# Kernel optimization log

Hardware: AMD Instinct MI355X
Metric: run time of the kernel (lower is better)

The kernel has to match this reference:

```python
import jax, jax.numpy as jnp
import numpy as np

NUM_BANDS, B, K, D = 5, 512, 64, 200
H = 4            # num attention heads
HID = 512        # selector hidden width
S = 0.02         # weight init scale


def setup_inputs() -> dict:
    key = jax.random.key(0)
    ks = jax.random.split(key, 8)
    F_IN = NUM_BANDS * K * D  # 64000
    return {
        "bands": jax.random.normal(ks[0], (NUM_BANDS, B, K, D), jnp.float32),
        "w1": jax.random.normal(ks[1], (HID, F_IN), jnp.float32) * S,
        "b1": jnp.zeros((HID,), jnp.float32),
        "w2": jax.random.normal(ks[2], (NUM_BANDS, HID), jnp.float32) * S,
        "b2": jnp.zeros((NUM_BANDS,), jnp.float32),
        "in_proj_w": jax.random.normal(ks[3], (3 * D, D), jnp.float32) * S,
        "in_proj_b": jnp.zeros((3 * D,), jnp.float32),
        "out_w": jax.random.normal(ks[4], (D, D), jnp.float32) * S,
        "out_b": jnp.zeros((D,), jnp.float32),
    }


def reference(bands, w1, b1, w2, b2, in_proj_w, in_proj_b, out_w, out_b):
    nb, Bb, k, d = bands.shape
    hd = d // H
    scale = 1.0 / np.sqrt(hd)

    # concat(bands, dim=1): [B, nb*k, d] in band-major order
    x = jnp.transpose(bands, (1, 0, 2, 3))           # [B, nb, k, d]
    kv_in = x.reshape(Bb, nb * k, d)                 # [B, nb*k, d]

    # router MLP + softmax + argmax band select
    flat = kv_in.reshape(Bb, -1)                     # [B, nb*k*d]
    h = jax.nn.relu(flat @ w1.T + b1)                # [B, HID]
    band_weights = jax.nn.softmax(h @ w2.T + b2, axis=-1)
    sel = jnp.argmax(band_weights, axis=-1)          # [B] int

    # gather selected band per sample as the query
    Q = bands[sel, jnp.arange(Bb)]                   # [B, k, d]

    # multihead cross-attention (torch nn.MultiheadAttention math)
    wq, wk, wv = jnp.split(in_proj_w, 3, axis=0)
    bq, bk, bv = jnp.split(in_proj_b, 3, axis=0)
    q = (Q @ wq.T + bq).reshape(Bb, k, H, hd).transpose(0, 2, 1, 3)        # [B,H,k,hd]
    kk = (kv_in @ wk.T + bk).reshape(Bb, nb * k, H, hd).transpose(0, 2, 1, 3)
    v = (kv_in @ wv.T + bv).reshape(Bb, nb * k, H, hd).transpose(0, 2, 1, 3)

    attn = jax.nn.softmax(jnp.einsum('bhqe,bhke->bhqk', q, kk) * scale, axis=-1)
    o = jnp.einsum('bhqk,bhke->bhqe', attn, v)       # [B,H,k,hd]
    o = o.transpose(0, 2, 1, 3).reshape(Bb, k, d)
    return o @ out_w.T + out_b                        # [B, k, d]
```

## Files before the change

### kernel.cpp

```cpp
#include <hip/hip_runtime.h>
#include <hip/hip_bf16.h>

#define NBANDS 5
#define BATCH  512
#define KQN    64
#define DM     200
#define NHEAD  4
#define HD     50
#define HIDW   512
#define TKV    320
#define FIN    64000
#define BSTRIDE 6553600
#define KSPLIT 40
#define KCH    1600
#define RCH    25
#define NTT    13
#define KST    7
#define NTKV   25

typedef __bf16  bf16x8 __attribute__((ext_vector_type(8)));
typedef float   f32x4  __attribute__((ext_vector_type(4)));

static __device__ inline unsigned short f2bf(float f) {
    __hip_bfloat16 h = __float2bfloat16(f);
    return *reinterpret_cast<unsigned short*>(&h);
}
static __device__ inline float bf2f(unsigned short u) {
    union { unsigned int i; float f; } x;
    x.i = ((unsigned int)u) << 16;
    return x.f;
}
static __device__ inline bf16x8 bf8zero() {
    union { bf16x8 v; unsigned int u[4]; } z;
    z.u[0] = z.u[1] = z.u[2] = z.u[3] = 0u;
    return z.v;
}
static __device__ inline void split8(const float4& a, const float4& b,
                                     bf16x8& hi, bf16x8& lo) {
    union { bf16x8 v; unsigned short u[8]; } H, L;
    const float xs[8] = {a.x, a.y, a.z, a.w, b.x, b.y, b.z, b.w};
#pragma unroll
    for (int i = 0; i < 8; ++i) {
        H.u[i] = f2bf(xs[i]);
        L.u[i] = f2bf(xs[i] - bf2f(H.u[i]));
    }
    hi = H.v; lo = L.v;
}
static __device__ inline bf16x8 round8(const float4& a, const float4& b) {
    union { bf16x8 v; unsigned short u[8]; } H;
    const float xs[8] = {a.x, a.y, a.z, a.w, b.x, b.y, b.z, b.w};
#pragma unroll
    for (int i = 0; i < 8; ++i) H.u[i] = f2bf(xs[i]);
    return H.v;
}

__global__ __launch_bounds__(256) void k_splitw1(
    const float* __restrict__ w1, unsigned short* __restrict__ BHp,
    unsigned short* __restrict__ BLp)
{
    __shared__ __align__(16) unsigned short Hs[128][72];
    __shared__ __align__(16) unsigned short Ls[128][72];
    const int kc = blockIdx.x;
    const int jt = blockIdx.y;
    const int t  = threadIdx.x;
    const int rl0 = t >> 4, cl4 = (t & 15) * 4;
#pragma unroll
    for (int i = 0; i < 8; ++i) {
        const int row = rl0 + i * 16;
        const float4 v = *(const float4*)(w1
            + (size_t)(jt * 128 + row) * FIN + kc * 64 + cl4);
        ushort4 hh, ll;
        hh.x = f2bf(v.x); ll.x = f2bf(v.x - bf2f(hh.x));
        hh.y = f2bf(v.y); ll.y = f2bf(v.y - bf2f(hh.y));
        hh.z = f2bf(v.z); ll.z = f2bf(v.z - bf2f(hh.z));
        hh.w = f2bf(v.w); ll.w = f2bf(v.w - bf2f(hh.w));
        *(ushort4*)&Hs[row][cl4] = hh;
        *(ushort4*)&Ls[row][cl4] = ll;
    }
    __syncthreads();
    const size_t tbase = ((size_t)(jt * 1000 + kc)) << 13;
#pragma unroll
    for (int i = 0; i < 4; ++i) {
        const int slot = i * 256 + t;
        const int ksnt = slot >> 6, lane = slot & 63;
        const int ks = ksnt >> 3, nt = ksnt & 7;
        const int row = nt * 16 + (lane & 15);
        const int col = ks * 32 + (lane >> 4) * 8;
        *(uint4*)(BHp + tbase + (size_t)slot * 8) = *(const uint4*)&Hs[row][col];
        *(uint4*)(BLp + tbase + (size_t)slot * 8) = *(const uint4*)&Ls[row][col];
    }
}

__global__ __launch_bounds__(256, 2) void k_router_mfma(
    const float* __restrict__ bands, const unsigned short* __restrict__ BHp,
    const unsigned short* __restrict__ BLp, float* __restrict__ part)
{
    __shared__ __align__(16) unsigned short BsH[2][8192];
    __shared__ __align__(16) unsigned short BsL[2][8192];

    const int lin = (blockIdx.z << 5) | (blockIdx.y << 2) | blockIdx.x;
    const int logical = (lin & 7) * 160 + (lin >> 3);
    const int z   = logical >> 5;
    const int rem = logical & 31;
    const int bt  = rem >> 2, jt = rem & 3;
    const int b0  = bt << 6, j0 = jt << 7;

    const int t = threadIdx.x;
    const int w = t >> 6, lane = t & 63;
    const int lm = lane & 15, quad = lane >> 4;
    const int m0 = w << 4;

    const float* xrow = bands + (size_t)(z >> 3) * BSTRIDE
                      + (size_t)(b0 + m0 + lm) * 12800 + (z & 7) * KCH
                      + quad * 8;
    const size_t tile0 = ((size_t)(jt * 1000 + z * RCH)) << 13;

    auto stage = [&](int chunk, int buf) {
        const unsigned short* srcH = BHp + tile0 + ((size_t)chunk << 13);
        const unsigned short* srcL = BLp + tile0 + ((size_t)chunk << 13);
#pragma unroll
        for (int pass = 0; pass < 4; ++pass) {
            const int i = pass * 256 + t;
            __builtin_amdgcn_global_load_lds(
                (const __attribute__((address_space(1))) unsigned int*)(srcH + (size_t)i * 8),
                (__attribute__((address_space(3))) unsigned int*)&BsH[buf][(pass * 256 + w * 64) * 8],
                16, 0, 0);
            __builtin_amdgcn_global_load_lds(
                (const __attribute__((address_space(1))) unsigned int*)(srcL + (size_t)i * 8),
                (__attribute__((address_space(3))) unsigned int*)&BsL[buf][(pass * 256 + w * 64) * 8],
                16, 0, 0);
        }
    };

    f32x4 acc[8];
#pragma unroll
    for (int nt = 0; nt < 8; ++nt) acc[nt] = (f32x4){0.f, 0.f, 0.f, 0.f};

    stage(0, 0);
    __syncthreads();
    for (int chunk = 0; chunk < RCH; ++chunk) {
        const int buf = chunk & 1;
        if (chunk + 1 < RCH) stage(chunk + 1, buf ^ 1);
        const float* ap = xrow + chunk * 64;
        const float4 a00 = *(const float4*)(ap);
        const float4 a01 = *(const float4*)(ap + 4);
        const float4 a10 = *(const float4*)(ap + 32);
        const float4 a11 = *(const float4*)(ap + 36);
        bf16x8 ah0, al0, ah1, al1;
        split8(a00, a01, ah0, al0);
        split8(a10, a11, ah1, al1);
        const unsigned short* hc = &BsH[buf][lane * 8];
        const unsigned short* lc = &BsL[buf][lane * 8];
#pragma unroll
        for (int nt = 0; nt < 8; ++nt) {
            const bf16x8 bh = *(const bf16x8*)(hc + (nt << 9));
            const bf16x8 bl = *(const bf16x8*)(lc + (nt << 9));
            acc[nt] = __builtin_amdgcn_mfma_f32_16x16x32_bf16(ah0, bh, acc[nt], 0, 0, 0);
            acc[nt] = __builtin_amdgcn_mfma_f32_16x16x32_bf16(al0, bh, acc[nt], 0, 0, 0);
            acc[nt] = __builtin_amdgcn_mfma_f32_16x16x32_bf16(ah0, bl, acc[nt], 0, 0, 0);
        }
#pragma unroll
        for (int nt = 0; nt < 8; ++nt) {
            const bf16x8 bh = *(const bf16x8*)(hc + ((8 + nt) << 9));
            const bf16x8 bl = *(const bf16x8*)(lc + ((8 + nt) << 9));
            acc[nt] = __builtin_amdgcn_mfma_f32_16x16x32_bf16(ah1, bh, acc[nt], 0, 0, 0);
            acc[nt] = __builtin_amdgcn_mfma_f32_16x16x32_bf16(al1, bh, acc[nt], 0, 0, 0);
            acc[nt] = __builtin_amdgcn_mfma_f32_16x16x32_bf16(ah1, bl, acc[nt], 0, 0, 0);
        }
        __syncthreads();
    }
    float* po = part + (size_t)z * (BATCH * HIDW);
#pragma unroll
    for (int nt = 0; nt < 8; ++nt) {
        const int jj = j0 + nt * 16 + lm;
#pragma unroll
        for (int reg = 0; reg < 4; ++reg) {
            const int bb = b0 + m0 + quad * 4 + reg;
            po[(size_t)bb * HIDW + jj] = acc[nt][reg];
        }
    }
}

__global__ __launch_bounds__(256) void k_reduce_relu(
    const float* __restrict__ part, const float* __restrict__ b1,
    float* __restrict__ h)
{
    const int tid = blockIdx.x * 256 + threadIdx.x;
    float s = b1[tid & (HIDW - 1)];
#pragma unroll 8
    for (int z = 0; z < KSPLIT; ++z) s += part[z * (BATCH * HIDW) + tid];
    h[tid] = fmaxf(s, 0.f);
}

__global__ __launch_bounds__(256) void k_wpack(
    const float* __restrict__ ipw, const float* __restrict__ outw,
    unsigned short* __restrict__ WqHp, unsigned short* __restrict__ WqLp,
    unsigned short* __restrict__ OwHp, unsigned short* __restrict__ OwLp)
{
    const int p = blockIdx.x;
    const int ks = p / NTT, nt = p - ks * NTT;
    const int t = threadIdx.x;
    const int lane = t >> 2, e0 = (t & 3) * 2;
    const int lm = lane & 15, quad = lane >> 4;
    const int row = nt * 16 + lm;
    const int k  = ks * 32 + quad * 8 + e0;
    const float* src = (blockIdx.y == 0) ? ipw : outw;
    unsigned short* dh = (blockIdx.y == 0) ? WqHp : OwHp;
    unsigned short* dl = (blockIdx.y == 0) ? WqLp : OwLp;
    float v0 = 0.f, v1 = 0.f;
    if (row < DM && k < DM) {
        v0 = src[(size_t)row * DM + k];
        v1 = src[(size_t)row * DM + k + 1];
    }
    const int off = (p << 9) + (lane << 3) + e0;
    const unsigned short h0 = f2bf(v0), h1 = f2bf(v1);
    dh[off]     = h0;
    dh[off + 1] = h1;
    dl[off]     = f2bf(v0 - bf2f(h0));
    dl[off + 1] = f2bf(v1 - bf2f(h1));
}

__global__ __launch_bounds__(256) void k_wpack_kv(
    const float* __restrict__ ipw, unsigned short* __restrict__ Wkv)
{
    const int p = blockIdx.x;
    const int ks = p / NTKV, nt = p - ks * NTKV;
    const int t = threadIdx.x;
    const int lane = t >> 2, e0 = (t & 3) * 2;
    const int lm = lane & 15, quad = lane >> 4;
    const int row = nt * 16 + lm;
    const int k  = ks * 32 + quad * 8 + e0;
    float v0 = 0.f, v1 = 0.f;
    if (k < DM) {
        v0 = ipw[(size_t)(DM + row) * DM + k];
        v1 = ipw[(size_t)(DM + row) * DM + k + 1];
    }
    const int off = (p << 9) + (lane << 3) + e0;
    Wkv[off]     = f2bf(v0);
    Wkv[off + 1] = f2bf(v1);
}

__global__ __launch_bounds__(256) void k_argmax(
    const float* __restrict__ h, const float* __restrict__ w2,
    const float* __restrict__ b2, int* __restrict__ sel)
{
    __shared__ float red[NBANDS][256];
    const int b = blockIdx.x, t = threadIdx.x;
    float acc[NBANDS] = {0.f, 0.f, 0.f, 0.f, 0.f};
    for (int j = t; j < HIDW; j += 256) {
        const float hv = h[b * HIDW + j];
#pragma unroll
        for (int n = 0; n < NBANDS; ++n)
            acc[n] = fmaf(hv, w2[n * HIDW + j], acc[n]);
    }
#pragma unroll
    for (int n = 0; n < NBANDS; ++n) red[n][t] = acc[n];
    __syncthreads();
    for (int s = 128; s > 0; s >>= 1) {
        if (t < s) {
#pragma unroll
            for (int n = 0; n < NBANDS; ++n) red[n][t] += red[n][t + s];
        }
        __syncthreads();
    }
    if (t == 0) {
        int best = 0;
        float bv = red[0][0] + b2[0];
        for (int n = 1; n < NBANDS; ++n) {
            const float v = red[n][0] + b2[n];
            if (v > bv) { bv = v; best = n; }
        }
        sel[b] = best;
    }
}

template<bool BF16OUT>
static __device__ inline void proj_core(
    const float* __restrict__ x0,
    const unsigned short* __restrict__ Ph,
    const unsigned short* __restrict__ Pl,
    const float* __restrict__ bias,
    void* __restrict__ outp)
{
    const int t = threadIdx.x;
    const int w = t >> 6, lane = t & 63;
    const int lm = lane & 15, quad = lane >> 4;
    const int m0 = w * 16;
    const float* xrow = x0 + (size_t)(m0 + lm) * DM;

    f32x4 acc[NTT];
#pragma unroll
    for (int nt = 0; nt < NTT; ++nt) acc[nt] = (f32x4){0.f, 0.f, 0.f, 0.f};

#pragma unroll
    for (int ks = 0; ks < KST; ++ks) {
        const int k0 = ks * 32 + quad * 8;
        bf16x8 a_h = bf8zero(), a_l = bf8zero();
        if (k0 + 8 <= DM) {
            const float4 xa = *(const float4*)(xrow + k0);
            const float4 xb = *(const float4*)(xrow + k0 + 4);
            split8(xa, xb, a_h, a_l);
        }
        const unsigned short* ph = Ph + ((ks * NTT) << 9) + (lane << 3);
        const unsigned short* pl = Pl + ((ks * NTT) << 9) + (lane << 3);
#pragma unroll
        for (int nt = 0; nt < NTT; ++nt) {
            const bf16x8 b_h = *(const bf16x8*)(ph + (nt << 9));
            const bf16x8 b_l = *(const bf16x8*)(pl + (nt << 9));
            acc[nt] = __builtin_amdgcn_mfma_f32_16x16x32_bf16(a_h, b_h, acc[nt], 0, 0, 0);
            acc[nt] = __builtin_amdgcn_mfma_f32_16x16x32_bf16(a_l, b_h, acc[nt], 0, 0, 0);
            acc[nt] = __builtin_amdgcn_mfma_f32_16x16x32_bf16(a_h, b_l, acc[nt], 0, 0, 0);
        }
    }
#pragma unroll
    for (int nt = 0; nt < NTT; ++nt) {
        const int col = nt * 16 + lm;
        if (col < DM) {
            const float bs = bias[col];
#pragma unroll
            for (int reg = 0; reg < 4; ++reg) {
                const int row = m0 + quad * 4 + reg;
                const float v = acc[nt][reg] + bs;
                if (BF16OUT)
                    ((unsigned short*)outp)[(size_t)row * DM + col] = f2bf(v);
                else
                    ((float*)outp)[(size_t)row * DM + col] = v;
            }
        }
    }
}

__global__ __launch_bounds__(256) void k_qproj_mfma(
    const float* __restrict__ bands, const int* __restrict__ sel,
    const unsigned short* __restrict__ WqHp, const unsigned short* __restrict__ WqLp,
    const float* __restrict__ ipb, unsigned short* __restrict__ qb)
{
    const int b = blockIdx.x;
    const int band = sel[b];
    const float* x0 = bands + (size_t)((band * BATCH + b) * KQN) * DM;
    proj_core<true>(x0, WqHp, WqLp, ipb, qb + (size_t)(b * KQN) * DM);
}

__global__ __launch_bounds__(256) void k_outproj_mfma(
    const float* __restrict__ obuf, const unsigned short* __restrict__ OwHp,
    const unsigned short* __restrict__ OwLp, const float* __restrict__ outb,
    float* __restrict__ out)
{
    const int b = blockIdx.x;
    proj_core<false>(obuf + (size_t)(b * KQN) * DM, OwHp, OwLp, outb,
                     out + (size_t)(b * KQN) * DM);
}

__global__ __launch_bounds__(256) void k_kvproj_lds(
    const float* __restrict__ bands, const unsigned short* __restrict__ Wkv,
    const float* __restrict__ ipb, __hip_bfloat16* __restrict__ Kp,
    __hip_bfloat16* __restrict__ Vp)
{
    __shared__ __align__(16) unsigned short Bs[2][NTKV * 512];
    const int t = threadIdx.x;
    const int w = t >> 6, lane = t & 63;
    const int lm = lane & 15, quad = lane >> 4;
    const int m0 = w * 16;
    const int M0 = blockIdx.x * 64;

    const int gg = M0 + m0 + lm;
    const int bb = gg / TKV, tk = gg - bb * TKV;
    const int band = tk >> 6, kk = tk & 63;
    const float* xrow = bands + (size_t)((band * BATCH + bb) * KQN + kk) * DM;

    float4 ar[2 * KST];
#pragma unroll
    for (int ks = 0; ks < KST; ++ks) {
        const int k0 = ks * 32 + quad * 8;
        if (k0 + 8 <= DM) {
            ar[2 * ks]     = *(const float4*)(xrow + k0);
            ar[2 * ks + 1] = *(const float4*)(xrow + k0 + 4);
        }
    }
    bf16x8 a[KST];
#pragma unroll
    for (int ks = 0; ks < KST; ++ks) {
        const int k0 = ks * 32 + quad * 8;
        a[ks] = (k0 + 8 <= DM) ? round8(ar[2 * ks], ar[2 * ks + 1]) : bf8zero();
    }

    auto stage = [&](int ks, int buf) {
        const unsigned short* src = Wkv + ((ks * NTKV) << 9);
#pragma unroll
        for (int pass = 0; pass < 6; ++pass) {
            const int i = pass * 256 + t;
            __builtin_amdgcn_global_load_lds(
                (const __attribute__((address_space(1))) unsigned int*)(src + (size_t)i * 8),
                (__attribute__((address_space(3))) unsigned int*)&Bs[buf][(pass * 256 + w * 64) * 8],
                16, 0, 0);
        }
        if (t < 64) {
            __builtin_amdgcn_global_load_lds(
                (const __attribute__((address_space(1))) unsigned int*)(src + (size_t)(1536 + lane) * 8),
                (__attribute__((address_space(3))) unsigned int*)&Bs[buf][1536 * 8],
                16, 0, 0);
        }
    };

    f32x4 acc[NTKV];
#pragma unroll
    for (int nt = 0; nt < NTKV; ++nt) acc[nt] = (f32x4){0.f, 0.f, 0.f, 0.f};

    stage(0, 0);
    __syncthreads();
#pragma unroll
    for (int ks = 0; ks < KST; ++ks) {
        if (ks + 1 < KST) stage(ks + 1, (ks + 1) & 1);
        const unsigned short* bs = &Bs[ks & 1][lane * 8];
#pragma unroll
        for (int nt = 0; nt < NTKV; ++nt) {
            const bf16x8 b8 = *(const bf16x8*)(bs + (nt << 9));
            acc[nt] = __builtin_amdgcn_mfma_f32_16x16x32_bf16(a[ks], b8, acc[nt], 0, 0, 0);
        }
        __syncthreads();
    }

#pragma unroll
    for (int nt = 0; nt < NTKV; ++nt) {
        const int col = nt * 16 + lm;
        const float bias = ipb[DM + col];
#pragma unroll
        for (int reg = 0; reg < 4; ++reg) {
            const int grow = M0 + m0 + quad * 4 + reg;
            const float v = acc[nt][reg] + bias;
            if (col < DM) Kp[(size_t)grow * DM + col] = __float2bfloat16(v);
            else          Vp[(size_t)grow * DM + (col - DM)] = __float2bfloat16(v);
        }
    }
}

__global__ __launch_bounds__(256) void k_attn(
    const unsigned short* __restrict__ qb, const __hip_bfloat16* __restrict__ Kp,
    const __hip_bfloat16* __restrict__ Vp, float* __restrict__ obuf)
{
    __shared__ __align__(16) unsigned short Qs[64][72];
    __shared__ __align__(16) unsigned short KP[320][72];
    __shared__ __align__(16) unsigned short Vt[64][328];
    __shared__ __align__(16) unsigned short Ps[64][328];
    const int b = blockIdx.x, hh = blockIdx.y;
    const int t = threadIdx.x;

    const unsigned short* qbase = qb + (size_t)(b * KQN) * DM + hh * HD;
    for (int idx = t; idx < 64 * 64; idx += 256) {
        const int r = idx >> 6, e = idx & 63;
        Qs[r][e] = (e < HD) ? qbase[(size_t)r * DM + e] : 0;
    }
    const unsigned short* kbase = (const unsigned short*)Kp + (size_t)b * TKV * DM + hh * HD;
    for (int idx = t; idx < 320 * 25; idx += 256) {
        const int key = idx / 25, g = idx - key * 25;
        *(unsigned int*)&KP[key][g * 2] =
            *(const unsigned int*)(kbase + (size_t)key * DM + g * 2);
    }
    for (int idx = t; idx < 320 * 7; idx += 256) {
        const int key = idx / 7, g = idx - key * 7;
        *(unsigned int*)&KP[key][50 + g * 2] = 0;
    }
    const unsigned short* vbase = (const unsigned short*)Vp + (size_t)b * TKV * DM + hh * HD;
    for (int idx = t; idx < 320 * 25; idx += 256) {
        const int key = idx / 25, g = idx - key * 25;
        const unsigned int v = *(const unsigned int*)(vbase + (size_t)key * DM + g * 2);
        Vt[g * 2][key]     = (unsigned short)(v & 0xffffu);
        Vt[g * 2 + 1][key] = (unsigned short)(v >> 16);
    }
    __syncthreads();

    const int w = t >> 6, lane = t & 63;
    const int lm = lane & 15, quad = lane >> 4;
    const int m0 = w * 16;

    f32x4 s[20];
#pragma unroll
    for (int nt = 0; nt < 20; ++nt) s[nt] = (f32x4){0.f, 0.f, 0.f, 0.f};
#pragma unroll
    for (int ks = 0; ks < 2; ++ks) {
        const int ka = ks * 32 + quad * 8;
        const bf16x8 a = *(const bf16x8*)&Qs[m0 + lm][ka];
#pragma unroll
        for (int nt = 0; nt < 20; ++nt) {
            const bf16x8 bb8 = *(const bf16x8*)&KP[nt * 16 + lm][ka];
            s[nt] = __builtin_amdgcn_mfma_f32_16x16x32_bf16(a, bb8, s[nt], 0, 0, 0);
        }
    }

    const float scale = 0.14142135623730951f;
    float inv[4];
#pragma unroll
    for (int reg = 0; reg < 4; ++reg) {
        float mx = -1e30f;
#pragma unroll
        for (int nt = 0; nt < 20; ++nt) {
            const float sv = s[nt][reg] * scale;
            s[nt][reg] = sv;
            mx = fmaxf(mx, sv);
        }
#pragma unroll
        for (int off = 1; off < 16; off <<= 1)
            mx = fmaxf(mx, __shfl_xor(mx, off, 64));
        float lsum = 0.f;
#pragma unroll
        for (int nt = 0; nt < 20; ++nt) {
            const float p = __expf(s[nt][reg] - mx);
            s[nt][reg] = p;
            lsum += p;
        }
#pragma unroll
        for (int off = 1; off < 16; off <<= 1)
            lsum += __shfl_xor(lsum, off, 64);
        inv[reg] = 1.f / lsum;
    }
#pragma unroll
    for (int reg = 0; reg < 4; ++reg) {
        const int row = m0 + quad * 4 + reg;
#pragma unroll
        for (int nt = 0; nt < 20; ++nt)
            Ps[row][nt * 16 + lm] = f2bf(s[nt][reg]);
    }
    __syncthreads();

    f32x4 o[4];
#pragma unroll
    for (int nt = 0; nt < 4; ++nt) o[nt] = (f32x4){0.f, 0.f, 0.f, 0.f};
#pragma unroll
    for (int ks = 0; ks < 10; ++ks) {
        const int ka = ks * 32 + quad * 8;
        const bf16x8 a = *(const bf16x8*)&Ps[m0 + lm][ka];
#pragma unroll
        for (int nt = 0; nt < 4; ++nt) {
            const bf16x8 bb8 = *(const bf16x8*)&Vt[nt * 16 + lm][ka];
            o[nt] = __builtin_amdgcn_mfma_f32_16x16x32_bf16(a, bb8, o[nt], 0, 0, 0);
        }
    }
    float* op = obuf + (size_t)(b * KQN) * DM + hh * HD;
#pragma unroll
    for (int nt = 0; nt < 4; ++nt) {
        const int e = nt * 16 + lm;
        if (e < HD) {
#pragma unroll
            for (int reg = 0; reg < 4; ++reg) {
                const int row = m0 + quad * 4 + reg;
                op[(size_t)row * DM + e] = o[nt][reg] * inv[reg];
            }
        }
    }
}

extern "C" void kernel_launch(void* const* d_in, const int* in_sizes, int n_in,
                              void* d_out, int out_size, void* d_ws, size_t ws_size,
                              hipStream_t stream)
{
    const float* bands = (const float*)d_in[0];
    const float* w1    = (const float*)d_in[1];
    const float* b1    = (const float*)d_in[2];
    const float* w2    = (const float*)d_in[3];
    const float* b2    = (const float*)d_in[4];
    const float* ipw   = (const float*)d_in[5];
    const float* ipb   = (const float*)d_in[6];
    const float* outw  = (const float*)d_in[7];
    const float* outb  = (const float*)d_in[8];
    float* out = (float*)d_out;

    if (ws_size < (size_t)192940032) return;

    char* ws = (char*)d_ws;
    int*   sel  = (int*)  (ws + 0);
    unsigned short* BHp  = (unsigned short*)(ws + 4096);
    unsigned short* BLp  = (unsigned short*)(ws + 65540096);
    float* part = (float*)(ws + 131076096);
    float* h    = (float*)(ws + 173019136);
    unsigned short* qb   = (unsigned short*)(ws + 4096);
    __hip_bfloat16* Kp   = (__hip_bfloat16*)(ws + 26776832);
    __hip_bfloat16* Vp   = (__hip_bfloat16*)(ws + 92312832);
    float* obuf = (float*)(ws + 157848832);
    unsigned short* Wkv  = (unsigned short*)(ws + 184063232);
    unsigned short* WqHp = (unsigned short*)(ws + 184242432);
    unsigned short* WqLp = (unsigned short*)(ws + 184335616);
    unsigned short* OwHp = (unsigned short*)(ws + 184428800);
    unsigned short* OwLp = (unsigned short*)(ws + 184521984);

    k_wpack_kv<<<KST * NTKV, 256, 0, stream>>>(ipw, Wkv);
    k_wpack<<<dim3(KST * NTT, 2), 256, 0, stream>>>(ipw, outw, WqHp, WqLp, OwHp, OwLp);
    k_splitw1<<<dim3(1000, 4), 256, 0, stream>>>(w1, BHp, BLp);

    k_router_mfma<<<dim3(4, 8, KSPLIT), 256, 0, stream>>>(bands, BHp, BLp, part);
    k_reduce_relu<<<(BATCH * HIDW) / 256, 256, 0, stream>>>(part, b1, h);
    k_argmax<<<BATCH, 256, 0, stream>>>(h, w2, b2, sel);
    k_qproj_mfma<<<BATCH, 256, 0, stream>>>(bands, sel, WqHp, WqLp, ipb, qb);
    k_kvproj_lds<<<2560, 256, 0, stream>>>(bands, Wkv, ipb, Kp, Vp);
    k_attn<<<dim3(BATCH, NHEAD), 256, 0, stream>>>(qb, Kp, Vp, obuf);
    k_outproj_mfma<<<BATCH, 256, 0, stream>>>(obuf, OwHp, OwLp, outb, out);
}
```

Baseline: 870.6 us.

## Retile router GEMM to 128x128 block tiles with 2x2 warp layout

Changes the router MFMA kernel from 64-row by 128-column tiles to 128x128 tiles. Each warp now computes a 64x64 sub-tile (4 row-subtiles by 4 column-subtiles), and the K loop advances 32 elements per stage with half-size LDS buffers. Doubling the rows per block halves the number of blocks and reuses each staged w1 tile across twice as many batch rows, cutting global and LDS traffic for the weights. In exchange, each thread holds more accumulator registers and the launch bound is raised to 3 blocks per CU, which risks register spills or lower occupancy.

```diff
diff --git a/kernel.cpp b/kernel.cpp
--- a/kernel.cpp
+++ b/kernel.cpp
@@ -13,7 +13,7 @@
 #define BSTRIDE 6553600
 #define KSPLIT 40
 #define KCH    1600
-#define RCH    25
+#define RC32   50
 #define NTT    13
 #define KST    7
 #define NTKV   25
@@ -91,92 +91,97 @@
     }
 }
 
-__global__ __launch_bounds__(256, 2) void k_router_mfma(
+__global__ __launch_bounds__(256, 3) void k_router_mfma(
     const float* __restrict__ bands, const unsigned short* __restrict__ BHp,
     const unsigned short* __restrict__ BLp, float* __restrict__ part)
 {
-    __shared__ __align__(16) unsigned short BsH[2][8192];
-    __shared__ __align__(16) unsigned short BsL[2][8192];
-
-    const int lin = (blockIdx.z << 5) | (blockIdx.y << 2) | blockIdx.x;
-    const int logical = (lin & 7) * 160 + (lin >> 3);
-    const int z   = logical >> 5;
-    const int rem = logical & 31;
+    __shared__ __align__(16) unsigned short BsH[2][4096];
+    __shared__ __align__(16) unsigned short BsL[2][4096];
+
+    const int lin = (blockIdx.z << 4) | (blockIdx.y << 2) | blockIdx.x;
+    const int logical = (lin & 7) * 80 + (lin >> 3);
+    const int z   = logical >> 4;
+    const int rem = logical & 15;
     const int bt  = rem >> 2, jt = rem & 3;
-    const int b0  = bt << 6, j0 = jt << 7;
 
     const int t = threadIdx.x;
     const int w = t >> 6, lane = t & 63;
     const int lm = lane & 15, quad = lane >> 4;
-    const int m0 = w << 4;
-
-    const float* xrow = bands + (size_t)(z >> 3) * BSTRIDE
-                      + (size_t)(b0 + m0 + lm) * 12800 + (z & 7) * KCH
-                      + quad * 8;
-    const size_t tile0 = ((size_t)(jt * 1000 + z * RCH)) << 13;
-
-    auto stage = [&](int chunk, int buf) {
-        const unsigned short* srcH = BHp + tile0 + ((size_t)chunk << 13);
-        const unsigned short* srcL = BLp + tile0 + ((size_t)chunk << 13);
-#pragma unroll
-        for (int pass = 0; pass < 4; ++pass) {
+    const int wr = w >> 1, wc = w & 1;
+
+    const float* xbase = bands + (size_t)(z >> 3) * BSTRIDE
+                       + (size_t)(bt * 128 + wr * 64 + lm) * 12800
+                       + (z & 7) * KCH + quad * 8;
+    const unsigned short* hbase = BHp + ((size_t)(jt * 1000 + z * 25) << 13);
+    const unsigned short* lbase = BLp + ((size_t)(jt * 1000 + z * 25) << 13);
+
+    auto stage = [&](int c, int buf) {
+        const size_t off = ((size_t)(c >> 1) << 13) + ((size_t)(c & 1) << 12);
+        const unsigned short* sH = hbase + off;
+        const unsigned short* sL = lbase + off;
+#pragma unroll
+        for (int pass = 0; pass < 2; ++pass) {
             const int i = pass * 256 + t;
             __builtin_amdgcn_global_load_lds(
-                (const __attribute__((address_space(1))) unsigned int*)(srcH + (size_t)i * 8),
+                (const __attribute__((address_space(1))) unsigned int*)(sH + (size_t)i * 8),
                 (__attribute__((address_space(3))) unsigned int*)&BsH[buf][(pass * 256 + w * 64) * 8],
                 16, 0, 0);
             __builtin_amdgcn_global_load_lds(
-                (const __attribute__((address_space(1))) unsigned int*)(srcL + (size_t)i * 8),
+                (const __attribute__((address_space(1))) unsigned int*)(sL + (size_t)i * 8),
                 (__attribute__((address_space(3))) unsigned int*)&BsL[buf][(pass * 256 + w * 64) * 8],
                 16, 0, 0);
         }
     };
 
-    f32x4 acc[8];
-#pragma unroll
-    for (int nt = 0; nt < 8; ++nt) acc[nt] = (f32x4){0.f, 0.f, 0.f, 0.f};
+    f32x4 acc[4][4];
+#pragma unroll
+    for (int rs = 0; rs < 4; ++rs)
+#pragma unroll
+        for (int nt = 0; nt < 4; ++nt) acc[rs][nt] = (f32x4){0.f, 0.f, 0.f, 0.f};
 
     stage(0, 0);
     __syncthreads();
-    for (int chunk = 0; chunk < RCH; ++chunk) {
-        const int buf = chunk & 1;
-        if (chunk + 1 < RCH) stage(chunk + 1, buf ^ 1);
-        const float* ap = xrow + chunk * 64;
-        const float4 a00 = *(const float4*)(ap);
-        const float4 a01 = *(const float4*)(ap + 4);
-        const float4 a10 = *(const float4*)(ap + 32);
-        const float4 a11 = *(const float4*)(ap + 36);
-        bf16x8 ah0, al0, ah1, al1;
-        split8(a00, a01, ah0, al0);
-        split8(a10, a11, ah1, al1);
-        const unsigned short* hc = &BsH[buf][lane * 8];
-        const unsigned short* lc = &BsL[buf][lane * 8];
-#pragma unroll
-        for (int nt = 0; nt < 8; ++nt) {
+    for (int c = 0; c < RC32; ++c) {
+        const int buf = c & 1;
+        if (c + 1 < RC32) stage(c + 1, buf ^ 1);
+        float4 a0[4], a1[4];
+#pragma unroll
+        for (int rs = 0; rs < 4; ++rs) {
+            const float* ap = xbase + (size_t)(rs * 16) * 12800 + c * 32;
+            a0[rs] = *(const float4*)(ap);
+            a1[rs] = *(const float4*)(ap + 4);
+        }
+        bf16x8 ah[4], al[4];
+#pragma unroll
+        for (int rs = 0; rs < 4; ++rs) split8(a0[rs], a1[rs], ah[rs], al[rs]);
+        const unsigned short* hc = &BsH[buf][(wc * 4) * 512 + lane * 8];
+        const unsigned short* lc = &BsL[buf][(wc * 4) * 512 + lane * 8];
+#pragma unroll
+        for (int nt = 0; nt < 4; ++nt) {
             const bf16x8 bh = *(const bf16x8*)(hc + (nt << 9));
             const bf16x8 bl = *(const bf16x8*)(lc + (nt << 9));
-            acc[nt] = __builtin_amdgcn_mfma_f32_16x16x32_bf16(ah0, bh, acc[nt], 0, 0, 0);
-            acc[nt] = __builtin_amdgcn_mfma_f32_16x16x32_bf16(al0, bh, acc[nt], 0, 0, 0);
-            acc[nt] = __builtin_amdgcn_mfma_f32_16x16x32_bf16(ah0, bl, acc[nt], 0, 0, 0);
-        }
-#pragma unroll
-        for (int nt = 0; nt < 8; ++nt) {
-            const bf16x8 bh = *(const bf16x8*)(hc + ((8 + nt) << 9));
-            const bf16x8 bl = *(const bf16x8*)(lc + ((8 + nt) << 9));
-            acc[nt] = __builtin_amdgcn_mfma_f32_16x16x32_bf16(ah1, bh, acc[nt], 0, 0, 0);
-            acc[nt] = __builtin_amdgcn_mfma_f32_16x16x32_bf16(al1, bh, acc[nt], 0, 0, 0);
-            acc[nt] = __builtin_amdgcn_mfma_f32_16x16x32_bf16(ah1, bl, acc[nt], 0, 0, 0);
+#pragma unroll
+            for (int rs = 0; rs < 4; ++rs) {
+                acc[rs][nt] = __builtin_amdgcn_mfma_f32_16x16x32_bf16(ah[rs], bh, acc[rs][nt], 0, 0, 0);
+                acc[rs][nt] = __builtin_amdgcn_mfma_f32_16x16x32_bf16(al[rs], bh, acc[rs][nt], 0, 0, 0);
+                acc[rs][nt] = __builtin_amdgcn_mfma_f32_16x16x32_bf16(ah[rs], bl, acc[rs][nt], 0, 0, 0);
+            }
         }
         __syncthreads();
     }
     float* po = part + (size_t)z * (BATCH * HIDW);
-#pragma unroll
-    for (int nt = 0; nt < 8; ++nt) {
-        const int jj = j0 + nt * 16 + lm;
-#pragma unroll
-        for (int reg = 0; reg < 4; ++reg) {
-            const int bb = b0 + m0 + quad * 4 + reg;
-            po[(size_t)bb * HIDW + jj] = acc[nt][reg];
+    const int j0 = jt * 128 + wc * 64;
+    const int b0 = bt * 128 + wr * 64;
+#pragma unroll
+    for (int rs = 0; rs < 4; ++rs) {
+#pragma unroll
+        for (int nt = 0; nt < 4; ++nt) {
+            const int jj = j0 + nt * 16 + lm;
+#pragma unroll
+            for (int reg = 0; reg < 4; ++reg) {
+                const int bb = b0 + rs * 16 + quad * 4 + reg;
+                po[(size_t)bb * HIDW + jj] = acc[rs][nt][reg];
+            }
         }
     }
 }
@@ -586,7 +591,7 @@
     k_wpack<<<dim3(KST * NTT, 2), 256, 0, stream>>>(ipw, outw, WqHp, WqLp, OwHp, OwLp);
     k_splitw1<<<dim3(1000, 4), 256, 0, stream>>>(w1, BHp, BLp);
 
-    k_router_mfma<<<dim3(4, 8, KSPLIT), 256, 0, stream>>>(bands, BHp, BLp, part);
+    k_router_mfma<<<dim3(4, 4, KSPLIT), 256, 0, stream>>>(bands, BHp, BLp, part);
     k_reduce_relu<<<(BATCH * HIDW) / 256, 256, 0, stream>>>(part, b1, h);
     k_argmax<<<BATCH, 256, 0, stream>>>(h, w2, b2, sel);
     k_qproj_mfma<<<BATCH, 256, 0, stream>>>(bands, sel, WqHp, WqLp, ipb, qb);
```

New measurement: 861.0 us. About the same (-1.1%).
